# Kernel optimization log

Measured on AMD Instinct MI355X. Metric: run time of the kernel, lower is better.

The kernel has to match this reference:

```python
import jax, jax.numpy as jnp
import numpy as np

STEPS = 200
H = 0.5
N_POP = 100000.0
CLAMP = 100000.0
BATCH = 65536


def setup_inputs() -> dict:
    key = jax.random.key(0)
    k1, k2 = jax.random.split(key)
    # init state [B, 1, 4] = (S, E, I, R); positive values
    init = jax.random.uniform(k1, (BATCH, 1, 4), dtype=jnp.float32) * 1000.0
    # weights mirrors nn.Parameter([100000, 3, 6, 0, 0.5, 0.2, 0.25]) with small noise
    base = jnp.array([100000.0, 3.0, 6.0, 0.0, 0.5, 0.2, 0.25], dtype=jnp.float32)
    weights = base + 0.01 * jax.random.normal(k2, (7,), dtype=jnp.float32)
    return {"init": init, "weights": weights}


def reference(init, weights):
    A, B, C = weights[4], weights[5], weights[6]

    def step(x, _):
        # x: [B, 1, 4]
        s, e, i = x[:, 0, 0], x[:, 0, 1], x[:, 0, 2]
        infl = B * s * (e + i) / N_POP
        d = jnp.stack((-infl, infl - A * e, A * e - C * i, C * i), axis=-1)  # [B, 4]
        x_new = x + H * jnp.clip(d[:, None, :], -CLAMP, CLAMP)  # [B, 1, 4]
        return x_new, x_new

    _, outs = jax.lax.scan(step, init, None, length=STEPS)  # [steps, B, 1, 4]
    return jnp.moveaxis(outs, 0, 1)  # [B, steps, 1, 4]
```

## Files before the change

kernel.cpp:

```cpp
#include <hip/hip_runtime.h>

#define BATCH   65536
#define STEPS   200
#define TCHUNK  8
#define NCHUNK  (STEPS / TCHUNK)
#define BLK     64
#define LSTRIDE 36

__device__ __forceinline__ void step_and_stash(
    float4& x, float A, float B, float C, float invN,
    float* __restrict__ buf, int lane, int tt)
{
    float infl = B * x.x * (x.y + x.z) * invN;
    float ae = A * x.y;
    float ci = C * x.z;
    float d0 = -infl;
    float d1 = infl - ae;
    float d2 = ae - ci;
    float d3 = ci;
    d0 = fminf(fmaxf(d0, -100000.0f), 100000.0f);
    d1 = fminf(fmaxf(d1, -100000.0f), 100000.0f);
    d2 = fminf(fmaxf(d2, -100000.0f), 100000.0f);
    d3 = fminf(fmaxf(d3, -100000.0f), 100000.0f);
    x.x += 0.5f * d0;
    x.y += 0.5f * d1;
    x.z += 0.5f * d2;
    x.w += 0.5f * d3;
    *reinterpret_cast<float4*>(&buf[lane * LSTRIDE + tt * 4]) = x;
}

__device__ __forceinline__ void compute_chunk(
    float4& x, float A, float B, float C, float invN,
    float* __restrict__ buf, int lane)
{
    #pragma unroll
    for (int tt = 0; tt < TCHUNK; ++tt)
        step_and_stash(x, A, B, C, invN, buf, lane, tt);
}

__device__ __forceinline__ void flush_chunk(
    const float* __restrict__ buf, float4* __restrict__ outf4,
    int base_b, int bbase, int jj, int t0)
{
    float4 f[8];
    #pragma unroll
    for (int k = 0; k < 8; ++k) {
        const int bb = k * 8 + bbase;
        f[k] = *reinterpret_cast<const float4*>(&buf[bb * LSTRIDE + jj * 4]);
    }
    #pragma unroll
    for (int k = 0; k < 8; ++k) {
        const int bb = k * 8 + bbase;
        outf4[(size_t)(base_b + bb) * STEPS + t0 + jj] = f[k];
    }
}

__global__ __launch_bounds__(BLK) void seir_kernel(
    const float* __restrict__ init,
    const float* __restrict__ w,
    float* __restrict__ out)
{
    __shared__ float ldsA[BLK * LSTRIDE];
    __shared__ float ldsB[BLK * LSTRIDE];

    const int lane   = threadIdx.x;
    const int base_b = blockIdx.x * BLK;
    const int b      = base_b + lane;

    const int jj    = lane & 7;
    const int bbase = lane >> 3;

    const float A = w[4];
    const float B = w[5];
    const float C = w[6];
    const float invN = 1.0f / 100000.0f;

    float4 x = reinterpret_cast<const float4*>(init)[b];
    float4* outf4 = reinterpret_cast<float4*>(out);

    compute_chunk(x, A, B, C, invN, ldsA, lane);

    for (int c = 1; c < NCHUNK; c += 2) {
        flush_chunk(ldsA, outf4, base_b, bbase, jj, (c - 1) * TCHUNK);
        compute_chunk(x, A, B, C, invN, ldsB, lane);
        flush_chunk(ldsB, outf4, base_b, bbase, jj, c * TCHUNK);
        compute_chunk(x, A, B, C, invN, ldsA, lane);
    }
    flush_chunk(ldsA, outf4, base_b, bbase, jj, (NCHUNK - 1) * TCHUNK);
}

extern "C" void kernel_launch(void* const* d_in, const int* in_sizes, int n_in,
                              void* d_out, int out_size, void* d_ws, size_t ws_size,
                              hipStream_t stream) {
    const float* init = (const float*)d_in[0];
    const float* w    = (const float*)d_in[1];
    float* out        = (float*)d_out;

    seir_kernel<<<dim3(BATCH / BLK), dim3(BLK), 0, stream>>>(init, w, out);
}
```

Baseline: 203.9 us.

## Replicate recurrence across four waves and round-robin chunk output writes

```diff
diff --git a/kernel.cpp b/kernel.cpp
--- a/kernel.cpp
+++ b/kernel.cpp
@@ -4,12 +4,11 @@
 #define STEPS   200
 #define TCHUNK  8
 #define NCHUNK  (STEPS / TCHUNK)
-#define BLK     64
+#define REP     4
+#define BLK     (64 * REP)
 #define LSTRIDE 36
 
-__device__ __forceinline__ void step_and_stash(
-    float4& x, float A, float B, float C, float invN,
-    float* __restrict__ buf, int lane, int tt)
+__device__ __forceinline__ void seir_step(float4& x, float A, float B, float C, float invN)
 {
     float infl = B * x.x * (x.y + x.z) * invN;
     float ae = A * x.y;
@@ -26,33 +25,6 @@
     x.y += 0.5f * d1;
     x.z += 0.5f * d2;
     x.w += 0.5f * d3;
-    *reinterpret_cast<float4*>(&buf[lane * LSTRIDE + tt * 4]) = x;
-}
-
-__device__ __forceinline__ void compute_chunk(
-    float4& x, float A, float B, float C, float invN,
-    float* __restrict__ buf, int lane)
-{
-    #pragma unroll
-    for (int tt = 0; tt < TCHUNK; ++tt)
-        step_and_stash(x, A, B, C, invN, buf, lane, tt);
-}
-
-__device__ __forceinline__ void flush_chunk(
-    const float* __restrict__ buf, float4* __restrict__ outf4,
-    int base_b, int bbase, int jj, int t0)
-{
-    float4 f[8];
-    #pragma unroll
-    for (int k = 0; k < 8; ++k) {
-        const int bb = k * 8 + bbase;
-        f[k] = *reinterpret_cast<const float4*>(&buf[bb * LSTRIDE + jj * 4]);
-    }
-    #pragma unroll
-    for (int k = 0; k < 8; ++k) {
-        const int bb = k * 8 + bbase;
-        outf4[(size_t)(base_b + bb) * STEPS + t0 + jj] = f[k];
-    }
 }
 
 __global__ __launch_bounds__(BLK) void seir_kernel(
@@ -60,11 +32,12 @@
     const float* __restrict__ w,
     float* __restrict__ out)
 {
-    __shared__ float ldsA[BLK * LSTRIDE];
-    __shared__ float ldsB[BLK * LSTRIDE];
+    __shared__ float lds[REP][64 * LSTRIDE];
 
-    const int lane   = threadIdx.x;
-    const int base_b = blockIdx.x * BLK;
+    const int tid    = threadIdx.x;
+    const int wv     = tid >> 6;
+    const int lane   = tid & 63;
+    const int base_b = blockIdx.x * 64;
     const int b      = base_b + lane;
 
     const int jj    = lane & 7;
@@ -77,16 +50,33 @@
 
     float4 x = reinterpret_cast<const float4*>(init)[b];
     float4* outf4 = reinterpret_cast<float4*>(out);
+    float* buf = lds[wv];
 
-    compute_chunk(x, A, B, C, invN, ldsA, lane);
-
-    for (int c = 1; c < NCHUNK; c += 2) {
-        flush_chunk(ldsA, outf4, base_b, bbase, jj, (c - 1) * TCHUNK);
-        compute_chunk(x, A, B, C, invN, ldsB, lane);
-        flush_chunk(ldsB, outf4, base_b, bbase, jj, c * TCHUNK);
-        compute_chunk(x, A, B, C, invN, ldsA, lane);
+    for (int c = 0; c < NCHUNK; ++c) {
+        if ((c & (REP - 1)) == wv) {
+            #pragma unroll
+            for (int tt = 0; tt < TCHUNK; ++tt) {
+                seir_step(x, A, B, C, invN);
+                *reinterpret_cast<float4*>(&buf[lane * LSTRIDE + tt * 4]) = x;
+            }
+            const int t0 = c * TCHUNK;
+            float4 f[8];
+            #pragma unroll
+            for (int k = 0; k < 8; ++k) {
+                const int bb = k * 8 + bbase;
+                f[k] = *reinterpret_cast<const float4*>(&buf[bb * LSTRIDE + jj * 4]);
+            }
+            #pragma unroll
+            for (int k = 0; k < 8; ++k) {
+                const int bb = k * 8 + bbase;
+                outf4[(size_t)(base_b + bb) * STEPS + t0 + jj] = f[k];
+            }
+        } else {
+            #pragma unroll
+            for (int tt = 0; tt < TCHUNK; ++tt)
+                seir_step(x, A, B, C, invN);
+        }
     }
-    flush_chunk(ldsA, outf4, base_b, bbase, jj, (NCHUNK - 1) * TCHUNK);
 }
 
 extern "C" void kernel_launch(void* const* d_in, const int* in_sizes, int n_in,
@@ -96,5 +86,5 @@
     const float* w    = (const float*)d_in[1];
     float* out        = (float*)d_out;
 
-    seir_kernel<<<dim3(BATCH / BLK), dim3(BLK), 0, stream>>>(init, w, out);
+    seir_kernel<<<dim3(BATCH / 64), dim3(BLK), 0, stream>>>(init, w, out);
 }
```

Result: no change. 206.5 us (+1.3%).
